# Performance work log

Hardware: AMD Instinct MI355X
Metric: run time of the kernel (lower is better)

Reference implementation:

```python
import jax, jax.numpy as jnp
import numpy as np

B, SQ, SK, H, DH = 4, 4096, 462, 10, 64  # batch, img tokens, text tokens, heads, head dim


def setup_inputs() -> dict:
    key = jax.random.key(0)
    k1, k2, k3, k4, k5 = jax.random.split(key, 5)
    q = jax.random.normal(k1, (B, SQ, H * DH), dtype=jnp.float32)
    k = jax.random.normal(k2, (B, SK, H * DH), dtype=jnp.float32)
    v = jax.random.normal(k3, (B, SK, H * DH), dtype=jnp.float32)
    # mask_scale = H*W / sum(mask) in the original -> positive, >= 1
    mask_scale = 1.0 + 3.0 * jax.random.uniform(k4, (B, H, SQ, SK), dtype=jnp.float32)
    mask_bool = jax.random.randint(k5, (B, H, SQ, SK), 0, 2).astype(bool)
    # guarantee every query row attends to at least one key (avoid all -inf rows)
    mask_bool = mask_bool.at[..., 0].set(True)
    return {"q": q, "k": k, "v": v, "mask_bool": mask_bool,
            "mask_scale": mask_scale, "heads": H}


def reference(q, k, v, mask_bool, mask_scale, heads):
    b, sq, d = q.shape
    dh = d // heads
    # [b, s, h*dh] -> [b, h, s, dh]
    qh = q.reshape(b, sq, heads, dh).transpose(0, 2, 1, 3)
    kh = k.reshape(b, -1, heads, dh).transpose(0, 2, 1, 3)
    vh = v.reshape(b, -1, heads, dh).transpose(0, 2, 1, 3)
    scale = 1.0 / np.sqrt(dh).astype(np.float32)
    scores = jnp.einsum("bhqd,bhkd->bhqk", qh, kh) * scale
    scores = scores * mask_scale
    scores = jnp.where(mask_bool, scores, -jnp.inf)
    attn = jax.nn.softmax(scores, axis=-1)
    out = jnp.einsum("bhqk,bhkd->bhqd", attn, vh)
    return out.transpose(0, 2, 1, 3).reshape(b, sq, d)
```

## Files before the change

kernel.cpp:

```cpp
#include <hip/hip_runtime.h>

#define B_  4
#define SQ_ 4096
#define SK_ 462
#define H_  10
#define DH_ 64
#define D_  (H_ * DH_)

typedef _Float16 half8 __attribute__((ext_vector_type(8)));
typedef float floatx4 __attribute__((ext_vector_type(4)));

__global__ void detect_mask_fmt(const unsigned int* __restrict__ mb_dw,
                                int* __restrict__ flag) {
  __shared__ int s_float, s_byte;
  if (threadIdx.x == 0) { s_float = 0; s_byte = 0; }
  __syncthreads();
  int fl = 0, by = 0;
  for (int i = threadIdx.x; i < 1024; i += 256) {
    unsigned int x = mb_dw[i];
    if (x > 1u) {
      if (x == 0x3F800000u) fl = 1; else by = 1;
    }
  }
  if (fl) atomicOr(&s_float, 1);
  if (by) atomicOr(&s_byte, 1);
  __syncthreads();
  if (threadIdx.x == 0) flag[0] = s_float ? 2 : (s_byte ? 1 : 0);
}

__global__ __launch_bounds__(256)
void attn_fwd(const float* __restrict__ q, const float* __restrict__ k,
              const float* __restrict__ v, const void* __restrict__ mb,
              const float* __restrict__ msc, float* __restrict__ out,
              const int* __restrict__ flag) {
  __shared__ __align__(16) float    qs[64][65];
  __shared__ __align__(16) _Float16 ks[32][66];
  __shared__ __align__(16) _Float16 vts[64][34];
  __shared__ __align__(16) _Float16 ps[4][16][34];

  const int tid  = threadIdx.x;
  const int wave = tid >> 6;
  const int lane = tid & 63;
  const int l16  = lane & 15;
  const int g4   = lane >> 4;

  const int b  = blockIdx.z;
  const int h  = blockIdx.y;
  const int q0 = blockIdx.x * 64;
  const int fmt = flag[0];

  {
    const float* qbase = q + (size_t)(b * SQ_ + q0) * D_ + h * DH_;
    #pragma unroll
    for (int i = 0; i < 4; ++i) {
      int idx4 = tid + i * 256;
      int row  = idx4 >> 4;
      int d4   = (idx4 & 15) * 4;
      float4 val = *reinterpret_cast<const float4*>(qbase + (size_t)row * D_ + d4);
      qs[row][d4 + 0] = val.x; qs[row][d4 + 1] = val.y;
      qs[row][d4 + 2] = val.z; qs[row][d4 + 3] = val.w;
    }
  }
  __syncthreads();

  half8 aq[2];
  {
    int row = wave * 16 + l16;
    #pragma unroll
    for (int kk = 0; kk < 2; ++kk) {
      int dbase = kk * 32 + g4 * 8;
      #pragma unroll
      for (int j = 0; j < 8; ++j) aq[kk][j] = (_Float16)qs[row][dbase + j];
    }
  }

  floatx4 o_acc[4];
  floatx4 l_acc;
  #pragma unroll
  for (int nt = 0; nt < 4; ++nt)
    #pragma unroll
    for (int r = 0; r < 4; ++r) o_acc[nt][r] = 0.0f;
  #pragma unroll
  for (int r = 0; r < 4; ++r) l_acc[r] = 0.0f;

  float m2[4] = {-1e30f, -1e30f, -1e30f, -1e30f};

  unsigned int rowoff[4];
  #pragma unroll
  for (int r = 0; r < 4; ++r) {
    int qrow = q0 + wave * 16 + g4 * 4 + r;
    rowoff[r] = (unsigned int)((b * H_ + h) * SQ_ + qrow) * SK_;
  }

  half8 ones_f;
  #pragma unroll
  for (int j = 0; j < 8; ++j) ones_f[j] = (_Float16)1.0f;

  const float c2 = 0.18033688011112042f;

  const float* kbase = k + (size_t)(b * SK_) * D_ + h * DH_;
  const float* vbase = v + (size_t)(b * SK_) * D_ + h * DH_;

  const int KT = (SK_ + 31) / 32;
  for (int kt = 0; kt < KT; ++kt) {
    __syncthreads();

    #pragma unroll
    for (int i = 0; i < 2; ++i) {
      int idx4 = tid + i * 256;
      int key  = idx4 >> 4;
      int d4   = (idx4 & 15) * 4;
      int gk   = kt * 32 + key;
      int gkc  = gk < SK_ ? gk : SK_ - 1;
      bool okk = gk < SK_;
      float4 kvv = *reinterpret_cast<const float4*>(kbase + (size_t)gkc * D_ + d4);
      float4 vvv = *reinterpret_cast<const float4*>(vbase + (size_t)gkc * D_ + d4);
      ks[key][d4 + 0] = (_Float16)kvv.x; ks[key][d4 + 1] = (_Float16)kvv.y;
      ks[key][d4 + 2] = (_Float16)kvv.z; ks[key][d4 + 3] = (_Float16)kvv.w;
      vts[d4 + 0][key] = okk ? (_Float16)vvv.x : (_Float16)0.0f;
      vts[d4 + 1][key] = okk ? (_Float16)vvv.y : (_Float16)0.0f;
      vts[d4 + 2][key] = okk ? (_Float16)vvv.z : (_Float16)0.0f;
      vts[d4 + 3][key] = okk ? (_Float16)vvv.w : (_Float16)0.0f;
    }

    float mscv[2][4];
    int   mval[2][4];
    #pragma unroll
    for (int ct = 0; ct < 2; ++ct) {
      #pragma unroll
      for (int r = 0; r < 4; ++r) {
        int col = kt * 32 + ct * 16 + l16;
        int cc  = col < SK_ ? col : SK_ - 1;
        unsigned int idx = rowoff[r] + (unsigned int)cc;
        mscv[ct][r] = msc[idx];
        int mv;
        if (fmt == 1)      mv = ((const unsigned char*)mb)[idx] != 0;
        else if (fmt == 0) mv = ((const int*)mb)[idx] != 0;
        else               mv = ((const float*)mb)[idx] != 0.0f;
        mval[ct][r] = (col < SK_) ? mv : 0;
      }
    }
    __syncthreads();

    floatx4 s[2];
    #pragma unroll
    for (int ct = 0; ct < 2; ++ct)
      #pragma unroll
      for (int r = 0; r < 4; ++r) s[ct][r] = 0.0f;
    #pragma unroll
    for (int ct = 0; ct < 2; ++ct) {
      int key = ct * 16 + l16;
      #pragma unroll
      for (int kk = 0; kk < 2; ++kk) {
        half8 kb;
        int dbase = kk * 32 + g4 * 8;
        #pragma unroll
        for (int j = 0; j < 8; ++j) kb[j] = ks[key][dbase + j];
        s[ct] = __builtin_amdgcn_mfma_f32_16x16x32_f16(aq[kk], kb, s[ct], 0, 0, 0);
      }
    }

    float pv[2][4];
    #pragma unroll
    for (int r = 0; r < 4; ++r) {
      float s0 = s[0][r] * (c2 * mscv[0][r]);
      float s1 = s[1][r] * (c2 * mscv[1][r]);
      s0 = mval[0][r] ? s0 : -1e30f;
      s1 = mval[1][r] ? s1 : -1e30f;
      float mx = fmaxf(s0, s1);
      mx = fmaxf(mx, __shfl_xor(mx, 1));
      mx = fmaxf(mx, __shfl_xor(mx, 2));
      mx = fmaxf(mx, __shfl_xor(mx, 4));
      mx = fmaxf(mx, __shfl_xor(mx, 8));
      float mnew  = fmaxf(m2[r], mx);
      float alpha = exp2f(m2[r] - mnew);
      m2[r] = mnew;
      pv[0][r] = exp2f(s0 - mnew);
      pv[1][r] = exp2f(s1 - mnew);
      l_acc[r] *= alpha;
      #pragma unroll
      for (int nt = 0; nt < 4; ++nt) o_acc[nt][r] *= alpha;
    }

    #pragma unroll
    for (int ct = 0; ct < 2; ++ct)
      #pragma unroll
      for (int r = 0; r < 4; ++r)
        ps[wave][g4 * 4 + r][ct * 16 + l16] = (_Float16)pv[ct][r];
    asm volatile("s_waitcnt lgkmcnt(0)" ::: "memory");
    half8 pa;
    #pragma unroll
    for (int j = 0; j < 8; ++j) pa[j] = ps[wave][l16][g4 * 8 + j];

    #pragma unroll
    for (int nt = 0; nt < 4; ++nt) {
      half8 vb;
      int dim = nt * 16 + l16;
      #pragma unroll
      for (int j = 0; j < 8; ++j) vb[j] = vts[dim][g4 * 8 + j];
      o_acc[nt] = __builtin_amdgcn_mfma_f32_16x16x32_f16(pa, vb, o_acc[nt], 0, 0, 0);
    }
    l_acc = __builtin_amdgcn_mfma_f32_16x16x32_f16(pa, ones_f, l_acc, 0, 0, 0);
  }

  #pragma unroll
  for (int r = 0; r < 4; ++r) {
    float inv = 1.0f / l_acc[r];
    int qrow = q0 + wave * 16 + g4 * 4 + r;
    float* ob = out + (size_t)(b * SQ_ + qrow) * D_ + h * DH_;
    #pragma unroll
    for (int nt = 0; nt < 4; ++nt)
      ob[nt * 16 + l16] = o_acc[nt][r] * inv;
  }
}

extern "C" void kernel_launch(void* const* d_in, const int* in_sizes, int n_in,
                              void* d_out, int out_size, void* d_ws, size_t ws_size,
                              hipStream_t stream) {
  const float* q   = (const float*)d_in[0];
  const float* k   = (const float*)d_in[1];
  const float* v   = (const float*)d_in[2];
  const void*  mb  = d_in[3];
  const float* msc = (const float*)d_in[4];
  float* out = (float*)d_out;
  int*   flg = (int*)d_ws;

  detect_mask_fmt<<<1, 256, 0, stream>>>((const unsigned int*)mb, flg);
  dim3 grid(SQ_ / 64, H_, B_);
  attn_fwd<<<grid, 256, 0, stream>>>(q, k, v, mb, msc, out, flg);
}
```

Baseline: 780.1 us.

## Pre-convert K/V to fp16 in workspace, drop LDS staging, prefetch masks

A new pre-pass converts K to fp16 and V to transposed fp16, zero-padded to 480 keys, in the workspace. The attention loop now reads MFMA operands directly from global memory instead of staging K/V through shared memory, which removes both per-tile barriers. Q fragments are loaded straight from global, and the mask and scale for the next key tile are prefetched one iteration ahead, folded into a single scale value that is zero where masked. The mask format is chosen through template specialisation, and launch bounds request 3 blocks per CU. The cost is an extra kernel launch, workspace traffic, and higher register pressure from the prefetched values.

```diff
diff --git a/kernel.cpp b/kernel.cpp
--- a/kernel.cpp
+++ b/kernel.cpp
@@ -6,12 +6,18 @@
 #define H_  10
 #define DH_ 64
 #define D_  (H_ * DH_)
+#define SKP_ 480
+#define KT_  15
 
 typedef _Float16 half8 __attribute__((ext_vector_type(8)));
 typedef float floatx4 __attribute__((ext_vector_type(4)));
 
-__global__ void detect_mask_fmt(const unsigned int* __restrict__ mb_dw,
-                                int* __restrict__ flag) {
+#define K16_ELEMS ((size_t)B_ * H_ * SKP_ * DH_)
+#define WS_NEEDED (2 * K16_ELEMS * sizeof(_Float16))
+
+__device__ int g_mask_fmt;
+
+__global__ void detect_mask_fmt(const unsigned int* __restrict__ mb_dw) {
   __shared__ int s_float, s_byte;
   if (threadIdx.x == 0) { s_float = 0; s_byte = 0; }
   __syncthreads();
@@ -25,19 +31,64 @@
   if (fl) atomicOr(&s_float, 1);
   if (by) atomicOr(&s_byte, 1);
   __syncthreads();
-  if (threadIdx.x == 0) flag[0] = s_float ? 2 : (s_byte ? 1 : 0);
-}
-
-__global__ __launch_bounds__(256)
-void attn_fwd(const float* __restrict__ q, const float* __restrict__ k,
-              const float* __restrict__ v, const void* __restrict__ mb,
-              const float* __restrict__ msc, float* __restrict__ out,
-              const int* __restrict__ flag) {
-  __shared__ __align__(16) float    qs[64][65];
-  __shared__ __align__(16) _Float16 ks[32][66];
-  __shared__ __align__(16) _Float16 vts[64][34];
-  __shared__ __align__(16) _Float16 ps[4][16][34];
-
+  if (threadIdx.x == 0) g_mask_fmt = s_float ? 2 : (s_byte ? 1 : 0);
+}
+
+__device__ __forceinline__ half8 cvt8(float4 a, float4 b) {
+  half8 o;
+  o[0] = (_Float16)a.x; o[1] = (_Float16)a.y;
+  o[2] = (_Float16)a.z; o[3] = (_Float16)a.w;
+  o[4] = (_Float16)b.x; o[5] = (_Float16)b.y;
+  o[6] = (_Float16)b.z; o[7] = (_Float16)b.w;
+  return o;
+}
+
+__global__ void convert_kv(const float* __restrict__ k, const float* __restrict__ v,
+                           _Float16* __restrict__ k16, _Float16* __restrict__ vt16) {
+  int t = blockIdx.x * 256 + threadIdx.x;
+  const int NK = B_ * H_ * SKP_ * (DH_ / 8);
+  const int NV = B_ * H_ * DH_ * (SKP_ / 8);
+  if (t < NK) {
+    int d8  = t & 7;
+    int key = (t >> 3) % SKP_;
+    int bh  = t / (8 * SKP_);
+    int b = bh / H_, h = bh % H_;
+    half8 o;
+    if (key < SK_) {
+      const float* src = k + ((size_t)(b * SK_ + key)) * D_ + h * DH_ + d8 * 8;
+      float4 f0 = *reinterpret_cast<const float4*>(src);
+      float4 f1 = *reinterpret_cast<const float4*>(src + 4);
+      o = cvt8(f0, f1);
+    } else {
+      #pragma unroll
+      for (int j = 0; j < 8; ++j) o[j] = (_Float16)0.0f;
+    }
+    *reinterpret_cast<half8*>(k16 + ((size_t)bh * SKP_ + key) * DH_ + d8 * 8) = o;
+  } else if (t < NK + NV) {
+    int u  = t - NK;
+    int k8 = u % (SKP_ / 8);
+    int d  = (u / (SKP_ / 8)) % DH_;
+    int bh = u / ((SKP_ / 8) * DH_);
+    int b = bh / H_, h = bh % H_;
+    half8 o;
+    #pragma unroll
+    for (int j = 0; j < 8; ++j) {
+      int key = k8 * 8 + j;
+      o[j] = (key < SK_)
+               ? (_Float16)v[((size_t)(b * SK_ + key)) * D_ + h * DH_ + d]
+               : (_Float16)0.0f;
+    }
+    *reinterpret_cast<half8*>(vt16 + ((size_t)bh * DH_ + d) * SKP_ + k8 * 8) = o;
+  }
+}
+
+template<bool WS, bool MBYTE>
+__device__ __forceinline__ void attn_body(
+    const float* __restrict__ q, const float* __restrict__ k,
+    const float* __restrict__ v, const void* __restrict__ mb,
+    const float* __restrict__ msc, float* __restrict__ out,
+    const _Float16* __restrict__ k16, const _Float16* __restrict__ vt16,
+    _Float16 (&ps)[4][16][34]) {
   const int tid  = threadIdx.x;
   const int wave = tid >> 6;
   const int lane = tid & 63;
@@ -47,30 +98,16 @@
   const int b  = blockIdx.z;
   const int h  = blockIdx.y;
   const int q0 = blockIdx.x * 64;
-  const int fmt = flag[0];
-
-  {
-    const float* qbase = q + (size_t)(b * SQ_ + q0) * D_ + h * DH_;
-    #pragma unroll
-    for (int i = 0; i < 4; ++i) {
-      int idx4 = tid + i * 256;
-      int row  = idx4 >> 4;
-      int d4   = (idx4 & 15) * 4;
-      float4 val = *reinterpret_cast<const float4*>(qbase + (size_t)row * D_ + d4);
-      qs[row][d4 + 0] = val.x; qs[row][d4 + 1] = val.y;
-      qs[row][d4 + 2] = val.z; qs[row][d4 + 3] = val.w;
-    }
-  }
-  __syncthreads();
+  const int bh = b * H_ + h;
 
   half8 aq[2];
   {
-    int row = wave * 16 + l16;
+    const float* qp = q + ((size_t)(b * SQ_ + q0 + wave * 16 + l16)) * D_ + h * DH_;
     #pragma unroll
     for (int kk = 0; kk < 2; ++kk) {
-      int dbase = kk * 32 + g4 * 8;
-      #pragma unroll
-      for (int j = 0; j < 8; ++j) aq[kk][j] = (_Float16)qs[row][dbase + j];
+      float4 f0 = *reinterpret_cast<const float4*>(qp + kk * 32 + g4 * 8);
+      float4 f1 = *reinterpret_cast<const float4*>(qp + kk * 32 + g4 * 8 + 4);
+      aq[kk] = cvt8(f0, f1);
     }
   }
 
@@ -82,7 +119,6 @@
     for (int r = 0; r < 4; ++r) o_acc[nt][r] = 0.0f;
   #pragma unroll
   for (int r = 0; r < 4; ++r) l_acc[r] = 0.0f;
-
   float m2[4] = {-1e30f, -1e30f, -1e30f, -1e30f};
 
   unsigned int rowoff[4];
@@ -98,49 +134,78 @@
 
   const float c2 = 0.18033688011112042f;
 
+  const unsigned char* mbb = (const unsigned char*)mb;
+  const unsigned int*  mbd = (const unsigned int*)mb;
+
+  auto load_masks = [&](int kt_, float (&m_)[2][4]) {
+    #pragma unroll
+    for (int ct = 0; ct < 2; ++ct)
+      #pragma unroll
+      for (int r = 0; r < 4; ++r) {
+        int col = kt_ * 32 + ct * 16 + l16;
+        int cc  = col < SK_ ? col : SK_ - 1;
+        unsigned int idx = rowoff[r] + (unsigned int)cc;
+        float sc = msc[idx];
+        unsigned int mvv = MBYTE ? (unsigned int)mbb[idx] : mbd[idx];
+        m_[ct][r] = (mvv != 0u && col < SK_) ? sc : 0.0f;
+      }
+  };
+
+  float mC[2][4];
+  load_masks(0, mC);
+
+  const _Float16* kbase16 = k16 + (size_t)bh * SKP_ * DH_;
+  const _Float16* vbase16 = vt16 + (size_t)bh * DH_ * SKP_;
   const float* kbase = k + (size_t)(b * SK_) * D_ + h * DH_;
   const float* vbase = v + (size_t)(b * SK_) * D_ + h * DH_;
 
-  const int KT = (SK_ + 31) / 32;
-  for (int kt = 0; kt < KT; ++kt) {
-    __syncthreads();
-
-    #pragma unroll
-    for (int i = 0; i < 2; ++i) {
-      int idx4 = tid + i * 256;
-      int key  = idx4 >> 4;
-      int d4   = (idx4 & 15) * 4;
-      int gk   = kt * 32 + key;
-      int gkc  = gk < SK_ ? gk : SK_ - 1;
-      bool okk = gk < SK_;
-      float4 kvv = *reinterpret_cast<const float4*>(kbase + (size_t)gkc * D_ + d4);
-      float4 vvv = *reinterpret_cast<const float4*>(vbase + (size_t)gkc * D_ + d4);
-      ks[key][d4 + 0] = (_Float16)kvv.x; ks[key][d4 + 1] = (_Float16)kvv.y;
-      ks[key][d4 + 2] = (_Float16)kvv.z; ks[key][d4 + 3] = (_Float16)kvv.w;
-      vts[d4 + 0][key] = okk ? (_Float16)vvv.x : (_Float16)0.0f;
-      vts[d4 + 1][key] = okk ? (_Float16)vvv.y : (_Float16)0.0f;
-      vts[d4 + 2][key] = okk ? (_Float16)vvv.z : (_Float16)0.0f;
-      vts[d4 + 3][key] = okk ? (_Float16)vvv.w : (_Float16)0.0f;
-    }
-
-    float mscv[2][4];
-    int   mval[2][4];
-    #pragma unroll
-    for (int ct = 0; ct < 2; ++ct) {
-      #pragma unroll
-      for (int r = 0; r < 4; ++r) {
-        int col = kt * 32 + ct * 16 + l16;
-        int cc  = col < SK_ ? col : SK_ - 1;
-        unsigned int idx = rowoff[r] + (unsigned int)cc;
-        mscv[ct][r] = msc[idx];
-        int mv;
-        if (fmt == 1)      mv = ((const unsigned char*)mb)[idx] != 0;
-        else if (fmt == 0) mv = ((const int*)mb)[idx] != 0;
-        else               mv = ((const float*)mb)[idx] != 0.0f;
-        mval[ct][r] = (col < SK_) ? mv : 0;
+  for (int kt = 0; kt < KT_; ++kt) {
+    half8 kbf[2][2];
+    if constexpr (WS) {
+      const _Float16* kp = kbase16 + (size_t)(kt * 32) * DH_;
+      #pragma unroll
+      for (int ct = 0; ct < 2; ++ct)
+        #pragma unroll
+        for (int kk = 0; kk < 2; ++kk)
+          kbf[ct][kk] = *reinterpret_cast<const half8*>(
+              kp + (ct * 16 + l16) * DH_ + kk * 32 + g4 * 8);
+    } else {
+      #pragma unroll
+      for (int ct = 0; ct < 2; ++ct) {
+        int key = kt * 32 + ct * 16 + l16;
+        int kc  = key < SK_ ? key : SK_ - 1;
+        #pragma unroll
+        for (int kk = 0; kk < 2; ++kk) {
+          const float* kp = kbase + (size_t)kc * D_ + kk * 32 + g4 * 8;
+          float4 f0 = *reinterpret_cast<const float4*>(kp);
+          float4 f1 = *reinterpret_cast<const float4*>(kp + 4);
+          kbf[ct][kk] = cvt8(f0, f1);
+        }
       }
     }
-    __syncthreads();
+
+    half8 vbf[4];
+    if constexpr (WS) {
+      const _Float16* vp = vbase16 + kt * 32 + g4 * 8;
+      #pragma unroll
+      for (int nt = 0; nt < 4; ++nt)
+        vbf[nt] = *reinterpret_cast<const half8*>(vp + (size_t)(nt * 16 + l16) * SKP_);
+    } else {
+      #pragma unroll
+      for (int nt = 0; nt < 4; ++nt) {
+        int dim = nt * 16 + l16;
+        #pragma unroll
+        for (int j = 0; j < 8; ++j) {
+          int key = kt * 32 + g4 * 8 + j;
+          vbf[nt][j] = (key < SK_)
+                         ? (_Float16)vbase[(size_t)key * D_ + dim]
+                         : (_Float16)0.0f;
+        }
+      }
+    }
+
+    float mN[2][4];
+    if (kt + 1 < KT_) load_masks(kt + 1, mN);
 
     floatx4 s[2];
     #pragma unroll
@@ -148,25 +213,17 @@
       #pragma unroll
       for (int r = 0; r < 4; ++r) s[ct][r] = 0.0f;
     #pragma unroll
-    for (int ct = 0; ct < 2; ++ct) {
-      int key = ct * 16 + l16;
-      #pragma unroll
-      for (int kk = 0; kk < 2; ++kk) {
-        half8 kb;
-        int dbase = kk * 32 + g4 * 8;
-        #pragma unroll
-        for (int j = 0; j < 8; ++j) kb[j] = ks[key][dbase + j];
-        s[ct] = __builtin_amdgcn_mfma_f32_16x16x32_f16(aq[kk], kb, s[ct], 0, 0, 0);
-      }
-    }
-
-    float pv[2][4];
+    for (int ct = 0; ct < 2; ++ct)
+      #pragma unroll
+      for (int kk = 0; kk < 2; ++kk)
+        s[ct] = __builtin_amdgcn_mfma_f32_16x16x32_f16(aq[kk], kbf[ct][kk], s[ct], 0, 0, 0);
+
+    float pw[2][4];
     #pragma unroll
     for (int r = 0; r < 4; ++r) {
-      float s0 = s[0][r] * (c2 * mscv[0][r]);
-      float s1 = s[1][r] * (c2 * mscv[1][r]);
-      s0 = mval[0][r] ? s0 : -1e30f;
-      s1 = mval[1][r] ? s1 : -1e30f;
+      float sc0 = mC[0][r], sc1 = mC[1][r];
+      float s0 = (sc0 != 0.0f) ? s[0][r] * (c2 * sc0) : -1e30f;
+      float s1 = (sc1 != 0.0f) ? s[1][r] * (c2 * sc1) : -1e30f;
       float mx = fmaxf(s0, s1);
       mx = fmaxf(mx, __shfl_xor(mx, 1));
       mx = fmaxf(mx, __shfl_xor(mx, 2));
@@ -175,8 +232,8 @@
       float mnew  = fmaxf(m2[r], mx);
       float alpha = exp2f(m2[r] - mnew);
       m2[r] = mnew;
-      pv[0][r] = exp2f(s0 - mnew);
-      pv[1][r] = exp2f(s1 - mnew);
+      pw[0][r] = exp2f(s0 - mnew);
+      pw[1][r] = exp2f(s1 - mnew);
       l_acc[r] *= alpha;
       #pragma unroll
       for (int nt = 0; nt < 4; ++nt) o_acc[nt][r] *= alpha;
@@ -186,21 +243,23 @@
     for (int ct = 0; ct < 2; ++ct)
       #pragma unroll
       for (int r = 0; r < 4; ++r)
-        ps[wave][g4 * 4 + r][ct * 16 + l16] = (_Float16)pv[ct][r];
+        ps[wave][g4 * 4 + r][ct * 16 + l16] = (_Float16)pw[ct][r];
     asm volatile("s_waitcnt lgkmcnt(0)" ::: "memory");
     half8 pa;
     #pragma unroll
     for (int j = 0; j < 8; ++j) pa[j] = ps[wave][l16][g4 * 8 + j];
 
     #pragma unroll
-    for (int nt = 0; nt < 4; ++nt) {
-      half8 vb;
-      int dim = nt * 16 + l16;
-      #pragma unroll
-      for (int j = 0; j < 8; ++j) vb[j] = vts[dim][g4 * 8 + j];
-      o_acc[nt] = __builtin_amdgcn_mfma_f32_16x16x32_f16(pa, vb, o_acc[nt], 0, 0, 0);
-    }
+    for (int nt = 0; nt < 4; ++nt)
+      o_acc[nt] = __builtin_amdgcn_mfma_f32_16x16x32_f16(pa, vbf[nt], o_acc[nt], 0, 0, 0);
     l_acc = __builtin_amdgcn_mfma_f32_16x16x32_f16(pa, ones_f, l_acc, 0, 0, 0);
+
+    if (kt + 1 < KT_) {
+      #pragma unroll
+      for (int ct = 0; ct < 2; ++ct)
+        #pragma unroll
+        for (int r = 0; r < 4; ++r) mC[ct][r] = mN[ct][r];
+    }
   }
 
   #pragma unroll
@@ -212,6 +271,17 @@
     for (int nt = 0; nt < 4; ++nt)
       ob[nt * 16 + l16] = o_acc[nt][r] * inv;
   }
+}
+
+template<bool WS>
+__global__ __launch_bounds__(256, 3)
+void attn_fwd(const float* __restrict__ q, const float* __restrict__ k,
+              const float* __restrict__ v, const void* __restrict__ mb,
+              const float* __restrict__ msc, float* __restrict__ out,
+              const _Float16* __restrict__ k16, const _Float16* __restrict__ vt16) {
+  __shared__ __align__(16) _Float16 ps[4][16][34];
+  if (g_mask_fmt == 1) attn_body<WS, true >(q, k, v, mb, msc, out, k16, vt16, ps);
+  else                 attn_body<WS, false>(q, k, v, mb, msc, out, k16, vt16, ps);
 }
 
 extern "C" void kernel_launch(void* const* d_in, const int* in_sizes, int n_in,
@@ -223,9 +293,17 @@
   const void*  mb  = d_in[3];
   const float* msc = (const float*)d_in[4];
   float* out = (float*)d_out;
-  int*   flg = (int*)d_ws;
-
-  detect_mask_fmt<<<1, 256, 0, stream>>>((const unsigned int*)mb, flg);
+
+  detect_mask_fmt<<<1, 256, 0, stream>>>((const unsigned int*)mb);
+
+  _Float16* k16  = (_Float16*)d_ws;
+  _Float16* vt16 = k16 + K16_ELEMS;
+
   dim3 grid(SQ_ / 64, H_, B_);
-  attn_fwd<<<grid, 256, 0, stream>>>(q, k, v, mb, msc, out, flg);
-}
+  if (d_ws != nullptr && ws_size >= WS_NEEDED) {
+    convert_kv<<<1200, 256, 0, stream>>>(k, v, k16, vt16);
+    attn_fwd<true><<<grid, 256, 0, stream>>>(q, k, v, mb, msc, out, k16, vt16);
+  } else {
+    attn_fwd<false><<<grid, 256, 0, stream>>>(q, k, v, mb, msc, out, k16, vt16);
+  }
+}
```

After: 833.5 us. +6.8%, slower.
